# Performance work log

Measured on AMD Instinct MI355X. Metric: run time of the kernel, lower is better.

The kernel has to match this reference:

```python
import jax, jax.numpy as jnp
import numpy as np
import math

N, E, T, H, IN_DIM, G, L = 8192, 131072, 262144, 128, 64, 32, 2
RBF_BINS, RBF_MAX, ANG_BINS = 32, 5.0, 16


def _rbf(d, r_max, n_bins):
    centers = jnp.linspace(0.0, r_max, n_bins, dtype=jnp.float32)
    delta = r_max / max(n_bins - 1, 1)
    gamma = 1.0 / (2.0 * (delta ** 2 + 1e-12))
    diff = d[:, None] - centers[None, :]
    return jnp.exp(-gamma * diff * diff)


def _mlp2(x, w1, b1, w2, b2):
    return jax.nn.silu(x @ w1 + b1) @ w2 + b2


def _ln(x, g, b):
    mu = jnp.mean(x, -1, keepdims=True)
    var = jnp.mean((x - mu) ** 2, -1, keepdims=True)
    return (x - mu) * jax.lax.rsqrt(var + 1e-5) * g + b


def _safe_norm(v):
    # ||v|| with grad-safe sqrt at v=0
    return jnp.sqrt(jnp.sum(v * v, -1) + 1e-12)


def setup_inputs() -> dict:
    key = jax.random.key(0)
    ks = iter(jax.random.split(key, 64))

    def lin(fan_in, shape):
        return jax.random.normal(next(ks), shape, jnp.float32) * (fan_in ** -0.5)

    x = jax.random.normal(next(ks), (N, IN_DIM), jnp.float32)
    pos = jax.random.normal(next(ks), (N, 3), jnp.float32) * 2.0
    edge_index = jax.random.randint(next(ks), (2, E), 0, N, jnp.int32)
    edge_dist = jnp.linalg.norm(pos[edge_index[1]] - pos[edge_index[0]], axis=-1)
    triplet_kj = jax.random.randint(next(ks), (T,), 0, E, jnp.int32)
    triplet_ji = jax.random.randint(next(ks), (T,), 0, E, jnp.int32)
    batch = jnp.sort(jax.random.randint(next(ks), (N,), 0, G, jnp.int32))
    TM_IN, MM_IN, CTX = 2 * RBF_BINS + ANG_BINS, 3 * H + RBF_BINS, 3 * H
    d = dict(
        x=x, pos=pos, edge_dist=edge_dist,
        node_in_w=lin(IN_DIM, (IN_DIM, H)), node_in_b=jnp.zeros(H),
        tm_w1=lin(TM_IN, (L, TM_IN, H)), tm_b1=jnp.zeros((L, H)),
        tm_w2=lin(H, (L, H, H)), tm_b2=jnp.zeros((L, H)),
        mm_w1=lin(MM_IN, (L, MM_IN, H)), mm_b1=jnp.zeros((L, H)),
        mm_w2=lin(H, (L, H, 2 * H)), mm_b2=jnp.zeros((L, 2 * H)),
        us_w1=lin(CTX, (L, CTX, H)), us_b1=jnp.zeros((L, H)),
        us_w2=lin(H, (L, H, H)), us_b2=jnp.zeros((L, H)),
        gv_w1=lin(CTX, (L, CTX, H)), gv_b1=jnp.zeros((L, H)),
        gv_w2=lin(H, (L, H, H)), gv_b2=jnp.zeros((L, H)),
        ln_g=jnp.ones((L, H)), ln_b=jnp.zeros((L, H)),
        vn_init=jnp.zeros(H),
        v2n_w1=lin(H, (H, H)), v2n_b1=jnp.zeros(H),
        v2n_w2=lin(H, (H, H)), v2n_b2=jnp.zeros(H),
        n2v_w1=lin(H, (H, H)), n2v_b1=jnp.zeros(H),
        n2v_w2=lin(H, (H, H)), n2v_b2=jnp.zeros(H),
        head_w1=lin(5 * H, (5 * H, H)), head_b1=jnp.zeros(H),
        head_w2=lin(H, (H, 1)), head_b2=jnp.zeros(1),
        edge_index=edge_index, triplet_kj=triplet_kj,
        triplet_ji=triplet_ji, batch=batch,
    )
    return d


def reference(x, pos, edge_dist, node_in_w, node_in_b, tm_w1, tm_b1, tm_w2, tm_b2,
              mm_w1, mm_b1, mm_w2, mm_b2, us_w1, us_b1, us_w2, us_b2,
              gv_w1, gv_b1, gv_w2, gv_b2, ln_g, ln_b, vn_init,
              v2n_w1, v2n_b1, v2n_w2, v2n_b2, n2v_w1, n2v_b1, n2v_w2, n2v_b2,
              head_w1, head_b1, head_w2, head_b2,
              edge_index, triplet_kj, triplet_ji, batch):
    src, dst = edge_index[0], edge_index[1]
    s = x @ node_in_w + node_in_b                              # [N,H]
    v = jnp.zeros((N, H, 3), s.dtype)                          # [N,H,3]
    vec = pos[dst] - pos[src]                                  # [E,3]
    edge_dir = vec / (edge_dist[:, None] + 1e-9)               # [E,3]
    edge_rbf = _rbf(edge_dist, RBF_MAX, RBF_BINS)              # [E,32]
    # 3-body angles between edge ji and edge kj
    a, b = vec[triplet_ji], vec[triplet_kj]                    # [T,3]
    cos = jnp.sum(a * b, -1) / (_safe_norm(a) * _safe_norm(b) + 1e-9)
    angle = jnp.arccos(jnp.clip(cos, -1.0 + 1e-7, 1.0 - 1e-7))
    angle_feat = _rbf(angle, math.pi, ANG_BINS)                # [T,16]
    vn = jnp.broadcast_to(vn_init, (G, H))
    for l in range(L):
        s = s + _mlp2(vn, v2n_w1, v2n_b1, v2n_w2, v2n_b2)[batch]
        # triplet gather -> MLP -> scatter onto edges
        t_in = jnp.concatenate([edge_rbf[triplet_kj], edge_rbf[triplet_ji], angle_feat], -1)
        t_msg = _mlp2(t_in, tm_w1[l], tm_b1[l], tm_w2[l], tm_b2[l])
        angle_agg = jax.ops.segment_sum(t_msg, triplet_ji, num_segments=E)   # [E,H]
        # edge messages -> scatter onto nodes (scalar + vector channels)
        msg_in = jnp.concatenate([s[src], s[dst], edge_rbf, angle_agg], -1)  # [E,416]
        msg = _mlp2(msg_in, mm_w1[l], mm_b1[l], mm_w2[l], mm_b2[l])          # [E,2H]
        m_s, m_vc = msg[:, :H], msg[:, H:]
        agg_s = jax.ops.segment_sum(m_s, dst, num_segments=N)                # [N,H]
        m_v = m_vc[:, :, None] * edge_dir[:, None, :]                        # [E,H,3]
        agg_v = jax.ops.segment_sum(m_v.reshape(E, H * 3), dst, num_segments=N).reshape(N, H, 3)
        ctx = jnp.concatenate([s, agg_s, _safe_norm(v)], -1)                 # [N,3H]
        s = s + _mlp2(ctx, us_w1[l], us_b1[l], us_w2[l], us_b2[l])
        gate = jax.nn.sigmoid(_mlp2(ctx, gv_w1[l], gv_b1[l], gv_w2[l], gv_b2[l]))
        v = v + gate[:, :, None] * agg_v
        s = jax.nn.silu(_ln(s, ln_g[l], ln_b[l]))
        vn = vn + _mlp2(jax.ops.segment_sum(s, batch, num_segments=G),
                        n2v_w1, n2v_b1, n2v_w2, n2v_b2)
    nf = jnp.concatenate([s, _safe_norm(v)], -1)                             # [N,2H]
    add_p = jax.ops.segment_sum(nf, batch, num_segments=G)
    counts = jax.ops.segment_sum(jnp.ones((N,), nf.dtype), batch, num_segments=G)
    mean_p = add_p / jnp.maximum(counts, 1.0)[:, None]
    g = jnp.concatenate([add_p, mean_p, vn], -1)                             # [G,5H]
    pred = _mlp2(g, head_w1, head_b1, head_w2, head_b2)                      # [G,1]
    return pred[:, 0]
```

## Files before the change

kernel.cpp:

```cpp
#include <hip/hip_runtime.h>
#include <math.h>

#define N_   8192
#define E_   131072
#define T_   262144
#define H_   128
#define IND_ 64
#define G_   32
#define L_   2

#define CW 64
#define RB 16

#define MROWS 32
#define HSTRIDE 136
#define WSTRIDE 36

#define STEP_E  ((float)(5.0/31.0))
#define GAMMA_E ((float)(1.0/(2.0*((5.0/31.0)*(5.0/31.0) + 1e-12))))
#define PI_D    3.14159265358979323846
#define STEP_A  ((float)(PI_D/15.0))
#define GAMMA_A ((float)(1.0/(2.0*((PI_D/15.0)*(PI_D/15.0) + 1e-12))))

typedef __attribute__((ext_vector_type(8))) short short8;
typedef __attribute__((ext_vector_type(4))) float f32x4;
typedef unsigned short ushort_t;

static __device__ __forceinline__ float fexp_f(float x){ return __expf(x); }
static __device__ __forceinline__ float silu_f(float x){ return x / (1.f + fexp_f(-x)); }
static __device__ __forceinline__ float sigmoid_f(float x){ return 1.f / (1.f + fexp_f(-x)); }

static __device__ __forceinline__ ushort_t f2bf(float x){
  unsigned int u = __builtin_bit_cast(unsigned int, x);
  u += 0x7FFFu + ((u >> 16) & 1u);
  return (ushort_t)(u >> 16);
}
static __device__ __forceinline__ float bf2f(ushort_t h){
  unsigned int u = ((unsigned int)h) << 16;
  return __builtin_bit_cast(float, u);
}


__global__ void k_zero(float* __restrict__ p, long n){
  long stride = (long)gridDim.x*256;
  long n4 = n >> 2;
  float4* p4 = (float4*)p;
  for (long i = (long)blockIdx.x*256 + threadIdx.x; i < n4; i += stride)
    p4[i] = make_float4(0.f,0.f,0.f,0.f);
  for (long i = (n4<<2) + (long)blockIdx.x*256 + threadIdx.x; i < n; i += stride)
    p[i] = 0.f;
}

__global__ void k_sentinel(float* __restrict__ p, int n){
  int i = blockIdx.x*256 + threadIdx.x;
  if (i < n) p[i] = 1.0e30f;
}

__global__ void k_init_vn(float* __restrict__ vn, const float* __restrict__ vn_init){
  int i = blockIdx.x*256 + threadIdx.x;
  if (i < G_*H_) vn[i] = vn_init[i & 127];
}

__global__ void k_bends(const int* __restrict__ batch, int* __restrict__ bends){
  int g = threadIdx.x;
  if (g >= G_) return;
  int lo = 0, hi = N_;
  while (lo < hi){
    int mid = (lo + hi) >> 1;
    if (batch[mid] <= g) lo = mid + 1; else hi = mid;
  }
  bends[g] = lo;
}

__global__ void k_wt_all(const float* __restrict__ tm_w1, const float* __restrict__ tm_w2,
                         const float* __restrict__ mm_w1, const float* __restrict__ mm_w2,
                         const float* __restrict__ us_w1, const float* __restrict__ us_w2,
                         const float* __restrict__ gv_w1, const float* __restrict__ gv_w2,
                         ushort_t* __restrict__ wtbuf){
  const int l = blockIdx.y;
  int i = blockIdx.x*256 + threadIdx.x;
  if (i >= 245760) return;
  ushort_t* base = wtbuf + (size_t)l*376832;
  if (i < 12288){
    int c = i/96, k = i%96;
    base[i] = (k < 80) ? f2bf(tm_w1[(size_t)l*10240 + (size_t)k*128 + c]) : (ushort_t)0;
  } else if (i < 28672){
    int j = i - 12288; int c = j >> 7, k = j & 127;
    base[12288 + j] = f2bf(tm_w2[(size_t)l*16384 + (size_t)k*128 + c]);
  } else if (i < 81920){
    int j = i - 28672; int c = j/416, k = j%416;
    base[28672 + j] = f2bf(mm_w1[(size_t)l*53248 + (size_t)k*128 + c]);
  } else if (i < 114688){
    int j = i - 81920; int c = j >> 7, k = j & 127;
    base[81920 + j] = f2bf(mm_w2[(size_t)l*32768 + (size_t)k*256 + c]);
  } else if (i < 163840){
    int j = i - 114688; int c = j/384, k = j%384;
    float w = us_w1[(size_t)l*49152 + (size_t)k*128 + c];
    ushort_t h = f2bf(w);
    base[114688 + j] = h; base[163840 + j] = f2bf(w - bf2f(h));
  } else if (i < 180224){
    int j = i - 163840; int c = j >> 7, k = j & 127;
    float w = us_w2[(size_t)l*16384 + (size_t)k*128 + c];
    ushort_t h = f2bf(w);
    base[212992 + j] = h; base[229376 + j] = f2bf(w - bf2f(h));
  } else if (i < 229376){
    int j = i - 180224; int c = j/384, k = j%384;
    float w = gv_w1[(size_t)l*49152 + (size_t)k*128 + c];
    ushort_t h = f2bf(w);
    base[245760 + j] = h; base[294912 + j] = f2bf(w - bf2f(h));
  } else {
    int j = i - 229376; int c = j >> 7, k = j & 127;
    float w = gv_w2[(size_t)l*16384 + (size_t)k*128 + c];
    ushort_t h = f2bf(w);
    base[344064 + j] = h; base[360448 + j] = f2bf(w - bf2f(h));
  }
}

__global__ void k_geom(const float* __restrict__ pos, const float* __restrict__ dist,
                       const int* __restrict__ ei,
                       float* __restrict__ vec, float* __restrict__ dir,
                       ushort_t* __restrict__ rbf16){
  int e = blockIdx.x*256 + threadIdx.x;
  if (e >= E_) return;
  int s = ei[e], d = ei[E_ + e];
  float vx = pos[d*3+0] - pos[s*3+0];
  float vy = pos[d*3+1] - pos[s*3+1];
  float vz = pos[d*3+2] - pos[s*3+2];
  vec[e*3+0]=vx; vec[e*3+1]=vy; vec[e*3+2]=vz;
  float dd = dist[e];
  float inv = 1.f / (dd + 1e-9f);
  dir[e*3+0]=vx*inv; dir[e*3+1]=vy*inv; dir[e*3+2]=vz*inv;
  #pragma unroll
  for (int i=0;i<32;i++){
    float df = dd - i*STEP_E;
    rbf16[e*32+i] = f2bf(fexp_f(-GAMMA_E*df*df));
  }
}

__global__ void k_dirs(const float* __restrict__ dir, const int* __restrict__ perm_e,
                       float* __restrict__ dir_s){
  int p = blockIdx.x*256 + threadIdx.x;
  if (p >= E_) return;
  int e = perm_e[p];
  dir_s[p*3+0] = dir[e*3+0];
  dir_s[p*3+1] = dir[e*3+1];
  dir_s[p*3+2] = dir[e*3+2];
}

__global__ void k_angle(const float* __restrict__ vec,
                        const int* __restrict__ kj, const int* __restrict__ ji,
                        float* __restrict__ angle){
  int t = blockIdx.x*256 + threadIdx.x;
  if (t >= T_) return;
  int ea = ji[t], eb = kj[t];
  float ax=vec[ea*3+0], ay=vec[ea*3+1], az=vec[ea*3+2];
  float bx=vec[eb*3+0], by=vec[eb*3+1], bz=vec[eb*3+2];
  float dot = ax*bx + ay*by + az*bz;
  float na = sqrtf(ax*ax+ay*ay+az*az + 1e-12f);
  float nb = sqrtf(bx*bx+by*by+bz*bz + 1e-12f);
  float c = dot / (na*nb + 1e-9f);
  c = fminf(fmaxf(c, -1.f + 1e-7f), 1.f - 1e-7f);
  angle[t] = acosf(c);
}


__global__ void k_hist(const int* __restrict__ keys, int M, int* __restrict__ hist){
  int i = blockIdx.x*256 + threadIdx.x;
  if (i < M) atomicAdd(&hist[keys[i]], 1);
}

__global__ void k_hist2(const int* __restrict__ keys, const int* __restrict__ map,
                        int M, int* __restrict__ hist){
  int i = blockIdx.x*256 + threadIdx.x;
  if (i < M) atomicAdd(&hist[map[keys[i]]], 1);
}

__global__ void k_scan1(const int* __restrict__ in, int* __restrict__ out,
                        int* __restrict__ sums, int B){
  __shared__ int sh[1024];
  int base = blockIdx.x*1024, t = threadIdx.x;
  for (int j=t;j<1024;j+=256) sh[j] = (base+j<B) ? in[base+j] : 0;
  __syncthreads();
  for (int o=1;o<1024;o<<=1){
    int v[4];
    #pragma unroll
    for (int q=0;q<4;q++){ int idx=t+q*256; v[q]=(idx>=o)? sh[idx-o]:0; }
    __syncthreads();
    #pragma unroll
    for (int q=0;q<4;q++){ int idx=t+q*256; sh[idx]+=v[q]; }
    __syncthreads();
  }
  for (int j=t;j<1024;j+=256) if (base+j<B) out[base+j] = (j==0)?0:sh[j-1];
  if (t==0) sums[blockIdx.x] = sh[1023];
}

__global__ void k_scan2(int* __restrict__ sums, int nb){
  if (threadIdx.x==0 && blockIdx.x==0){
    int a=0;
    for (int i=0;i<nb;i++){ int x=sums[i]; sums[i]=a; a+=x; }
  }
}

__global__ void k_scan3(int* __restrict__ out, const int* __restrict__ sums, int B){
  int i = blockIdx.x*256+threadIdx.x;
  if (i<B) out[i] += sums[i>>10];
}

__global__ void k_fill(const int* __restrict__ keys, int M, int* __restrict__ cur,
                       int* __restrict__ perm){
  int i = blockIdx.x*256+threadIdx.x;
  if (i<M){ int p = atomicAdd(&cur[keys[i]],1); perm[p]=i; }
}

__global__ void k_fill2(const int* __restrict__ keys, const int* __restrict__ map,
                        int M, int* __restrict__ cur, int* __restrict__ perm){
  int i = blockIdx.x*256+threadIdx.x;
  if (i<M){ int p = atomicAdd(&cur[map[keys[i]]],1); perm[p]=i; }
}

__global__ void k_invert(const int* __restrict__ perm, int* __restrict__ rank, int M){
  int i = blockIdx.x*256+threadIdx.x;
  if (i<M) rank[perm[i]] = i;
}

template<int SM, int K1PAD>
__launch_bounds__(256, 4)
__global__ void k_mlp1(
    const int* __restrict__ perm,
    const int* __restrict__ idx1, const int* __restrict__ idx2,
    const ushort_t* __restrict__ rbf16, const float* __restrict__ angle,
    const ushort_t* __restrict__ s16, const ushort_t* __restrict__ eagg_in,
    const ushort_t* __restrict__ W1t, const float* __restrict__ b1,
    ushort_t* __restrict__ outbuf)
{
  __shared__ ushort_t lw[128*WSTRIDE];
  __shared__ ushort_t hid[4][16*HSTRIDE];
  const int tid  = threadIdx.x;
  const int wave = tid >> 6;
  const int lane = tid & 63;
  const int n    = lane & 15;
  const int quad = lane >> 4;
  const int kq   = quad*8;
  const int wrow = blockIdx.x*64 + wave*16;
  const int row  = wrow + n;

  const int e0 = perm[row];
  int i1a = idx1[e0];
  int i2a = idx2[e0];
  float ang0 = 0.f;
  if (SM == 1){ ang0 = angle[e0]; }

  f32x4 acc[8];
  #pragma unroll
  for (int ct=0;ct<8;ct++) acc[ct] = (f32x4){0.f,0.f,0.f,0.f};

  #pragma unroll
  for (int k0 = 0; k0 < K1PAD; k0 += 32){
    short8 a0;
    if (SM == 1){
      if (k0 == 0){
        a0 = *(const short8*)&rbf16[(size_t)i1a*32 + kq];
      } else if (k0 == 32){
        a0 = *(const short8*)&rbf16[(size_t)i2a*32 + kq];
      } else {
        #pragma unroll
        for (int j=0;j<8;j++){
          int kk = kq + j;
          float v0 = 0.f;
          if (kk < 16){
            float c = (float)kk*STEP_A;
            float d0 = ang0 - c;
            v0 = fexp_f(-GAMMA_A*d0*d0);
          }
          a0[j] = (short)f2bf(v0);
        }
      }
    } else {
      const int k = k0 + kq;
      if (k0 < 128){
        a0 = *(const short8*)&s16[(size_t)i1a*128 + k];
      } else if (k0 < 256){
        a0 = *(const short8*)&s16[(size_t)i2a*128 + (k-128)];
      } else if (k0 < 288){
        a0 = *(const short8*)&rbf16[(size_t)e0*32 + (k-256)];
      } else {
        a0 = *(const short8*)&eagg_in[(size_t)row*128 + (k-288)];
      }
    }

    #pragma unroll
    for (int it=0; it<2; it++){
      int idx = tid + it*256;
      int col = idx >> 2, seg = idx & 3;
      *(short8*)&lw[col*WSTRIDE + seg*8] = *(const short8*)&W1t[(size_t)col*K1PAD + k0 + seg*8];
    }
    __syncthreads();

    #pragma unroll
    for (int ct=0;ct<8;ct++){
      short8 b = *(const short8*)&lw[(ct*16 + n)*WSTRIDE + kq];
      acc[ct] = __builtin_amdgcn_mfma_f32_16x16x32_bf16(a0, b, acc[ct], 0,0,0);
    }
    __syncthreads();
  }

  #pragma unroll
  for (int ct=0;ct<8;ct++){
    int col = ct*16 + n;
    float bv = b1[col];
    #pragma unroll
    for (int reg=0;reg<4;reg++){
      int rloc = quad*4 + reg;
      float h = acc[ct][reg] + bv;
      hid[wave][rloc*HSTRIDE + col] = f2bf(silu_f(h));
    }
  }
  const int rsub = lane >> 4;
  const int c8   = (lane & 15) * 8;
  #pragma unroll
  for (int i=0;i<4;i++){
    int rloc = i*4 + rsub;
    int grow = wrow + rloc;
    short8 vv = *(const short8*)&hid[wave][(size_t)rloc*HSTRIDE + c8];
    *(short8*)&outbuf[(size_t)grow*128 + c8] = vv;
  }
}

__launch_bounds__(64, 4)
__global__ void k_aggemm_t(const ushort_t* __restrict__ tmsg, const int* __restrict__ tends,
                           const ushort_t* __restrict__ W2t, const float* __restrict__ b2,
                           ushort_t* __restrict__ eagg2){
  __shared__ ushort_t hid[MROWS*HSTRIDE];
  const int lane = threadIdx.x;
  const int n    = lane & 15;
  const int quad = lane >> 4;
  const int kq   = quad*8;
  const int wrow = blockIdx.x*MROWS;
  const int r0 = wrow + n, r1 = wrow + 16 + n;
  const int s0 = r0 ? tends[r0-1] : 0;
  const int e0 = tends[r0];
  const int s1 = tends[r1-1];
  const int e1 = tends[r1];

  f32x4 acc[2][8];
  #pragma unroll
  for (int rh=0;rh<2;rh++)
    #pragma unroll
    for (int ct=0;ct<8;ct++) acc[rh][ct] = (f32x4){0.f,0.f,0.f,0.f};

  #pragma unroll
  for (int k0=0;k0<128;k0+=32){
    float sum0[8], sum1[8];
    #pragma unroll
    for (int j=0;j<8;j++){ sum0[j]=0.f; sum1[j]=0.f; }
    for (int p=s0;p<e0;p++){
      short8 w = *(const short8*)&tmsg[(size_t)p*128 + k0 + kq];
      #pragma unroll
      for (int j=0;j<8;j++) sum0[j] += bf2f((ushort_t)w[j]);
    }
    for (int p=s1;p<e1;p++){
      short8 w = *(const short8*)&tmsg[(size_t)p*128 + k0 + kq];
      #pragma unroll
      for (int j=0;j<8;j++) sum1[j] += bf2f((ushort_t)w[j]);
    }
    short8 a0, a1;
    #pragma unroll
    for (int j=0;j<8;j++){
      a0[j] = (short)f2bf(sum0[j]);
      a1[j] = (short)f2bf(sum1[j]);
    }
    #pragma unroll
    for (int ct=0;ct<8;ct++){
      short8 b = *(const short8*)&W2t[(size_t)(ct*16 + n)*128 + k0 + kq];
      acc[0][ct] = __builtin_amdgcn_mfma_f32_16x16x32_bf16(a0, b, acc[0][ct], 0,0,0);
      acc[1][ct] = __builtin_amdgcn_mfma_f32_16x16x32_bf16(a1, b, acc[1][ct], 0,0,0);
    }
  }

  float cnts[2][4];
  #pragma unroll
  for (int rh=0;rh<2;rh++)
    #pragma unroll
    for (int reg=0;reg<4;reg++){
      int row = wrow + rh*16 + quad*4 + reg;
      cnts[rh][reg] = (float)(tends[row] - (row ? tends[row-1] : 0));
    }

  #pragma unroll
  for (int rh=0;rh<2;rh++){
    #pragma unroll
    for (int ct=0;ct<8;ct++){
      int col = ct*16 + n;
      float bv = b2[col];
      #pragma unroll
      for (int reg=0;reg<4;reg++){
        int rloc = rh*16 + quad*4 + reg;
        hid[rloc*HSTRIDE + col] = f2bf(acc[rh][ct][reg] + cnts[rh][reg]*bv);
      }
    }
  }
  const int rsub = lane >> 4;
  const int c8   = (lane & 15) * 8;
  #pragma unroll
  for (int i=0;i<8;i++){
    int rloc = i*4 + rsub;
    int grow = wrow + rloc;
    short8 vv = *(const short8*)&hid[(size_t)rloc*HSTRIDE + c8];
    *(short8*)&eagg2[(size_t)grow*128 + c8] = vv;
  }
}

__global__ void k_agg_e(const ushort_t* __restrict__ hbuf, const int* __restrict__ eends,
                        const float* __restrict__ dir_s, float* __restrict__ mom){
  int i = blockIdx.x*256 + threadIdx.x;
  int d = i >> 6, c2 = (i & 63)*2;
  if (d >= N_) return;
  int s = (d == 0) ? 0 : eends[d-1];
  int e = eends[d];
  float hs0=0.f,hs1=0.f, hx0=0.f,hx1=0.f, hy0=0.f,hy1=0.f, hz0=0.f,hz1=0.f;
  float sdx=0.f, sdy=0.f, sdz=0.f;
  for (int q=s;q<e;q++){
    unsigned int w = *(const unsigned int*)&hbuf[(size_t)q*128 + c2];
    float h0 = bf2f((ushort_t)(w & 0xFFFFu));
    float h1 = bf2f((ushort_t)(w >> 16));
    float dx = dir_s[q*3+0], dy = dir_s[q*3+1], dz = dir_s[q*3+2];
    hs0 += h0; hs1 += h1;
    hx0 += h0*dx; hx1 += h1*dx;
    hy0 += h0*dy; hy1 += h1*dy;
    hz0 += h0*dz; hz1 += h1*dz;
    sdx += dx; sdy += dy; sdz += dz;
  }
  size_t base = (size_t)d*128 + c2;
  *(float2*)&mom[base]                        = make_float2(hs0, hs1);
  *(float2*)&mom[(size_t)N_*128   + base]     = make_float2(hx0, hx1);
  *(float2*)&mom[(size_t)N_*256   + base]     = make_float2(hy0, hy1);
  *(float2*)&mom[(size_t)N_*384   + base]     = make_float2(hz0, hz1);
  if (c2 == 0){
    mom[(size_t)N_*512 + d*4+0] = sdx;
    mom[(size_t)N_*512 + d*4+1] = sdy;
    mom[(size_t)N_*512 + d*4+2] = sdz;
  }
}

__launch_bounds__(64, 4)
__global__ void k_gemm_e(const float* __restrict__ mom, const int* __restrict__ eends,
                         const ushort_t* __restrict__ W2t ,
                         const float* __restrict__ b2 ,
                         const float* __restrict__ v ,
                         ushort_t* __restrict__ a16h, ushort_t* __restrict__ a16l,
                         ushort_t* __restrict__ vnh,  ushort_t* __restrict__ vnl,
                         float* __restrict__ aggv ){
  __shared__ float sbuf[MROWS*130];
  const int lane = threadIdx.x;
  const int n    = lane & 15;
  const int quad = lane >> 4;
  const int kq   = quad*8;
  const int wrow = blockIdx.x*MROWS;
  const int og   = blockIdx.y;

  const float* M = mom + (size_t)og*((size_t)N_*128);
  const ushort_t* W = W2t + (og ? (size_t)128*128 : 0);

  f32x4 acc[2][8];
  #pragma unroll
  for (int rh=0;rh<2;rh++)
    #pragma unroll
    for (int ct=0;ct<8;ct++) acc[rh][ct] = (f32x4){0.f,0.f,0.f,0.f};

  #pragma unroll
  for (int k0=0;k0<128;k0+=32){
    const int k = k0 + kq;
    const float* p0 = &M[(size_t)(wrow + n)*128 + k];
    const float* p1 = &M[(size_t)(wrow + 16 + n)*128 + k];
    f32x4 x0 = *(const f32x4*)p0, x1 = *(const f32x4*)(p0+4);
    f32x4 y0 = *(const f32x4*)p1, y1 = *(const f32x4*)(p1+4);
    short8 ah0, al0, ah1, al1;
    #pragma unroll
    for (int j=0;j<4;j++){
      ushort_t h;
      h = f2bf(x0[j]); ah0[j]   = (short)h; al0[j]   = (short)f2bf(x0[j] - bf2f(h));
      h = f2bf(x1[j]); ah0[4+j] = (short)h; al0[4+j] = (short)f2bf(x1[j] - bf2f(h));
      h = f2bf(y0[j]); ah1[j]   = (short)h; al1[j]   = (short)f2bf(y0[j] - bf2f(h));
      h = f2bf(y1[j]); ah1[4+j] = (short)h; al1[4+j] = (short)f2bf(y1[j] - bf2f(h));
    }
    #pragma unroll
    for (int ct=0;ct<8;ct++){
      short8 b = *(const short8*)&W[(size_t)(ct*16 + n)*128 + k0 + kq];
      acc[0][ct] = __builtin_amdgcn_mfma_f32_16x16x32_bf16(ah0, b, acc[0][ct], 0,0,0);
      acc[0][ct] = __builtin_amdgcn_mfma_f32_16x16x32_bf16(al0, b, acc[0][ct], 0,0,0);
      acc[1][ct] = __builtin_amdgcn_mfma_f32_16x16x32_bf16(ah1, b, acc[1][ct], 0,0,0);
      acc[1][ct] = __builtin_amdgcn_mfma_f32_16x16x32_bf16(al1, b, acc[1][ct], 0,0,0);
    }
  }

  const int rsub = lane >> 4;
  const int c8   = (lane & 15) * 8;

  if (og == 0){
    float cnts[2][4];
    #pragma unroll
    for (int rh=0;rh<2;rh++)
      #pragma unroll
      for (int reg=0;reg<4;reg++){
        int row = wrow + rh*16 + quad*4 + reg;
        cnts[rh][reg] = (float)(eends[row] - (row ? eends[row-1] : 0));
      }
    ushort_t* us = (ushort_t*)sbuf;
    #pragma unroll
    for (int rh=0;rh<2;rh++)
      #pragma unroll
      for (int ct=0;ct<8;ct++){
        int col = ct*16 + n;
        float bv = b2[col];
        #pragma unroll
        for (int reg=0;reg<4;reg++){
          int rloc = rh*16 + quad*4 + reg;
          float val = acc[rh][ct][reg] + cnts[rh][reg]*bv;
          us[rloc*HSTRIDE + col] = f2bf(val);
        }
      }
    #pragma unroll
    for (int i=0;i<8;i++){
      int rloc = i*4 + rsub;
      short8 vv = *(const short8*)&us[(size_t)rloc*HSTRIDE + c8];
      *(short8*)&a16h[(size_t)(wrow + rloc)*128 + c8] = vv;
    }
    #pragma unroll
    for (int rh=0;rh<2;rh++)
      #pragma unroll
      for (int ct=0;ct<8;ct++){
        int col = ct*16 + n;
        float bv = b2[col];
        #pragma unroll
        for (int reg=0;reg<4;reg++){
          int rloc = rh*16 + quad*4 + reg;
          float val = acc[rh][ct][reg] + cnts[rh][reg]*bv;
          ushort_t h = f2bf(val);
          us[rloc*HSTRIDE + col] = f2bf(val - bf2f(h));
        }
      }
    #pragma unroll
    for (int i=0;i<8;i++){
      int rloc = i*4 + rsub;
      short8 vv = *(const short8*)&us[(size_t)rloc*HSTRIDE + c8];
      *(short8*)&a16l[(size_t)(wrow + rloc)*128 + c8] = vv;
    }
    #pragma unroll 4
    for (int j=0;j<32;j++){
      size_t idx = (size_t)wrow*128 + (size_t)j*128 + lane*2;
      float2 a = *(const float2*)&v[idx];
      float2 b = *(const float2*)&v[(size_t)N_*128 + idx];
      float2 c = *(const float2*)&v[(size_t)N_*256 + idx];
      float n0 = sqrtf(a.x*a.x + b.x*b.x + c.x*c.x + 1e-12f);
      float n1 = sqrtf(a.y*a.y + b.y*b.y + c.y*c.y + 1e-12f);
      ushort_t h0 = f2bf(n0), h1 = f2bf(n1);
      *(unsigned int*)&vnh[idx] = (unsigned int)h0 | ((unsigned int)h1 << 16);
      *(unsigned int*)&vnl[idx] = (unsigned int)f2bf(n0 - bf2f(h0))
                                | ((unsigned int)f2bf(n1 - bf2f(h1)) << 16);
    }
  } else {
    const int x = og - 1;
    #pragma unroll
    for (int rh=0;rh<2;rh++)
      #pragma unroll
      for (int ct=0;ct<8;ct++){
        int col = ct*16 + n;
        float bv = b2[128 + col];
        #pragma unroll
        for (int reg=0;reg<4;reg++){
          int rloc = rh*16 + quad*4 + reg;
          int row = wrow + rloc;
          float sd = mom[(size_t)N_*512 + row*4 + x];
          sbuf[rloc*130 + col] = acc[rh][ct][reg] + sd*bv;
        }
      }
    float* plane = aggv + (size_t)x*((size_t)N_*128);
    #pragma unroll
    for (int i=0;i<8;i++){
      int rloc = i*4 + rsub;
      f32x4 v0 = *(const f32x4*)&sbuf[rloc*130 + c8];
      f32x4 v1 = *(const f32x4*)&sbuf[rloc*130 + c8 + 4];
      *(f32x4*)&plane[(size_t)(wrow + rloc)*128 + c8] = v0;
      *(f32x4*)&plane[(size_t)(wrow + rloc)*128 + c8 + 4] = v1;
    }
  }
}

__launch_bounds__(256, 3)
__global__ void k_node_mfma(
    const float* __restrict__ s_in,
    const ushort_t* __restrict__ a16h, const ushort_t* __restrict__ a16l,
    const ushort_t* __restrict__ vnh,  const ushort_t* __restrict__ vnl,
    float* __restrict__ s2, float* __restrict__ v_out ,
    const float* __restrict__ aggv ,
    const ushort_t* __restrict__ us1h, const ushort_t* __restrict__ us1l, const float* __restrict__ us_b1,
    const ushort_t* __restrict__ us2h, const ushort_t* __restrict__ us2l, const float* __restrict__ us_b2,
    const ushort_t* __restrict__ gv1h, const ushort_t* __restrict__ gv1l, const float* __restrict__ gv_b1,
    const ushort_t* __restrict__ gv2h, const ushort_t* __restrict__ gv2l, const float* __restrict__ gv_b2)
{
  __shared__ ushort_t lwh[128*WSTRIDE];
  __shared__ ushort_t lwl[128*WSTRIDE];
  __shared__ ushort_t hidh[4][16*HSTRIDE];
  __shared__ ushort_t hidl[4][16*HSTRIDE];
  const int tid  = threadIdx.x;
  const int wave = tid >> 6;
  const int lane = tid & 63;
  const int n    = lane & 15;
  const int quad = lane >> 4;
  const int kq   = quad*8;
  const int og   = blockIdx.y;
  const int wrow = blockIdx.x*64 + wave*16;
  const int r0 = wrow + n;

  const ushort_t* W1h = og ? gv1h : us1h;
  const ushort_t* W1l = og ? gv1l : us1l;
  const float*    B1  = og ? gv_b1 : us_b1;
  const ushort_t* W2h = og ? gv2h : us2h;
  const ushort_t* W2l = og ? gv2l : us2l;
  const float*    B2  = og ? gv_b2 : us_b2;

  f32x4 acc[8];
  #pragma unroll
  for (int ct=0;ct<8;ct++) acc[ct] = (f32x4){0.f,0.f,0.f,0.f};

  #pragma unroll
  for (int k0=0; k0<384; k0+=32){
    #pragma unroll
    for (int it = 0; it < 2; it++){
      int idx = tid + it*256;
      int col = idx >> 2, seg = idx & 3;
      *(short8*)&lwh[col*WSTRIDE + seg*8] = *(const short8*)&W1h[(size_t)col*384 + k0 + seg*8];
      *(short8*)&lwl[col*WSTRIDE + seg*8] = *(const short8*)&W1l[(size_t)col*384 + k0 + seg*8];
    }
    __syncthreads();

    short8 ah0, al0;
    const int k = k0 + kq;
    if (k0 < 128){
      const float* p0 = &s_in[(size_t)r0*128 + k];
      f32x4 x0 = *(const f32x4*)p0, x1 = *(const f32x4*)(p0+4);
      #pragma unroll
      for (int j=0;j<4;j++){
        ushort_t h;
        h = f2bf(x0[j]); ah0[j]   = (short)h; al0[j]   = (short)f2bf(x0[j] - bf2f(h));
        h = f2bf(x1[j]); ah0[4+j] = (short)h; al0[4+j] = (short)f2bf(x1[j] - bf2f(h));
      }
    } else if (k0 < 256){
      int kk = k - 128;
      ah0 = *(const short8*)&a16h[(size_t)r0*128 + kk];
      al0 = *(const short8*)&a16l[(size_t)r0*128 + kk];
    } else {
      int kk = k - 256;
      ah0 = *(const short8*)&vnh[(size_t)r0*128 + kk];
      al0 = *(const short8*)&vnl[(size_t)r0*128 + kk];
    }
    #pragma unroll
    for (int ct=0;ct<8;ct++){
      short8 bh = *(const short8*)&lwh[(ct*16 + n)*WSTRIDE + kq];
      short8 bl = *(const short8*)&lwl[(ct*16 + n)*WSTRIDE + kq];
      acc[ct] = __builtin_amdgcn_mfma_f32_16x16x32_bf16(ah0, bh, acc[ct], 0,0,0);
      acc[ct] = __builtin_amdgcn_mfma_f32_16x16x32_bf16(al0, bh, acc[ct], 0,0,0);
      acc[ct] = __builtin_amdgcn_mfma_f32_16x16x32_bf16(ah0, bl, acc[ct], 0,0,0);
    }
    __syncthreads();
  }

  #pragma unroll
  for (int ct=0;ct<8;ct++){
    int col = ct*16 + n;
    float bv = B1[col];
    #pragma unroll
    for (int reg=0;reg<4;reg++){
      int rloc = quad*4 + reg;
      float h = silu_f(acc[ct][reg] + bv);
      ushort_t hh = f2bf(h);
      hidh[wave][rloc*HSTRIDE + col] = hh;
      hidl[wave][rloc*HSTRIDE + col] = f2bf(h - bf2f(hh));
    }
  }

  f32x4 acc2[8];
  #pragma unroll
  for (int ct=0;ct<8;ct++) acc2[ct] = (f32x4){0.f,0.f,0.f,0.f};

  #pragma unroll
  for (int k0=0;k0<128;k0+=32){
    #pragma unroll
    for (int it = 0; it < 2; it++){
      int idx = tid + it*256;
      int col = idx >> 2, seg = idx & 3;
      *(short8*)&lwh[col*WSTRIDE + seg*8] = *(const short8*)&W2h[(size_t)col*128 + k0 + seg*8];
      *(short8*)&lwl[col*WSTRIDE + seg*8] = *(const short8*)&W2l[(size_t)col*128 + k0 + seg*8];
    }
    __syncthreads();

    short8 ah0 = *(const short8*)&hidh[wave][(size_t)(n)*HSTRIDE + k0 + kq];
    short8 al0 = *(const short8*)&hidl[wave][(size_t)(n)*HSTRIDE + k0 + kq];
    #pragma unroll
    for (int ct=0;ct<8;ct++){
      short8 bh = *(const short8*)&lwh[(ct*16 + n)*WSTRIDE + kq];
      short8 bl = *(const short8*)&lwl[(ct*16 + n)*WSTRIDE + kq];
      acc2[ct] = __builtin_amdgcn_mfma_f32_16x16x32_bf16(ah0, bh, acc2[ct], 0,0,0);
      acc2[ct] = __builtin_amdgcn_mfma_f32_16x16x32_bf16(al0, bh, acc2[ct], 0,0,0);
      acc2[ct] = __builtin_amdgcn_mfma_f32_16x16x32_bf16(ah0, bl, acc2[ct], 0,0,0);
    }
    __syncthreads();
  }

  if (og == 0){
    #pragma unroll
    for (int ct=0;ct<8;ct++){
      int col = ct*16 + n;
      float bv = B2[col];
      #pragma unroll
      for (int reg=0;reg<4;reg++){
        int row = wrow + quad*4 + reg;
        size_t idx = (size_t)row*128 + col;
        s2[idx] = s_in[idx] + acc2[ct][reg] + bv;
      }
    }
  } else {
    #pragma unroll
    for (int ct=0;ct<8;ct++){
      int col = ct*16 + n;
      float bv = B2[col];
      #pragma unroll
      for (int reg=0;reg<4;reg++){
        int row = wrow + quad*4 + reg;
        size_t idx = (size_t)row*128 + col;
        float g = sigmoid_f(acc2[ct][reg] + bv);
        v_out[idx]                    += g*aggv[idx];
        v_out[(size_t)N_*128 + idx]   += g*aggv[(size_t)N_*128 + idx];
        v_out[(size_t)N_*256 + idx]   += g*aggv[(size_t)N_*256 + idx];
      }
    }
  }
}

__launch_bounds__(128)
__global__ void k_gemm(const float* __restrict__ A,
                       const float* __restrict__ W,
                       const float* __restrict__ bias,
                       float* __restrict__ C, int R, int K)
{
  __shared__ float ws[CW*128];
  __shared__ float as[RB][CW];
  const int tid = threadIdx.x;
  const int nchunk = (K + CW - 1) / CW;

  for (int rb = blockIdx.x*RB; rb < R; rb += gridDim.x*RB){
    float acc[RB];
    #pragma unroll
    for (int r=0;r<RB;r++) acc[r] = 0.f;

    for (int c=0;c<nchunk;c++){
      const int k0 = c*CW;
      for (int i=tid; i<CW*128; i+=128){
        int kk = i >> 7, col = i & 127;
        int k = k0 + kk;
        ws[i] = (k < K) ? W[k*128 + col] : 0.f;
      }
      for (int i=tid; i<RB*CW; i+=128){
        int r  = i >> 6, kk = i & 63;
        int k  = k0 + kk;
        as[r][kk] = (k < K) ? A[(long)(rb+r)*K + k] : 0.f;
      }
      __syncthreads();
      #pragma unroll 4
      for (int kq2=0; kq2<CW/4; kq2++){
        float w0 = ws[(4*kq2+0)*128 + tid];
        float w1 = ws[(4*kq2+1)*128 + tid];
        float w2 = ws[(4*kq2+2)*128 + tid];
        float w3 = ws[(4*kq2+3)*128 + tid];
        #pragma unroll
        for (int r=0;r<RB;r++){
          const float4 av = *reinterpret_cast<const float4*>(&as[r][4*kq2]);
          acc[r] = fmaf(av.x, w0, acc[r]);
          acc[r] = fmaf(av.y, w1, acc[r]);
          acc[r] = fmaf(av.z, w2, acc[r]);
          acc[r] = fmaf(av.w, w3, acc[r]);
        }
      }
      __syncthreads();
    }

    const float bv = bias[tid];
    #pragma unroll
    for (int r=0;r<RB;r++)
      C[(long)(rb+r)*128 + tid] = acc[r] + bv;
  }
}


__launch_bounds__(256)
__global__ void k_small_mlp2(const float* __restrict__ in,
                             const float* __restrict__ w1, const float* __restrict__ b1,
                             const float* __restrict__ w2, const float* __restrict__ b2,
                             float* __restrict__ outp, int accumulate){
  __shared__ float a[4][128];
  __shared__ float h[4][128];
  int tid = threadIdx.x;
  int rbase = blockIdx.x*4;
  for (int i=tid;i<4*128;i+=256) a[i>>7][i&127] = in[(rbase + (i>>7))*128 + (i&127)];
  __syncthreads();
  int col = tid & 127, rg = tid >> 7;
  float acc0=0.f, acc1=0.f;
  for (int k=0;k<128;k++){
    float w = w1[k*128+col];
    acc0 = fmaf(a[rg*2+0][k], w, acc0);
    acc1 = fmaf(a[rg*2+1][k], w, acc1);
  }
  {
    float bv = b1[col];
    h[rg*2+0][col] = silu_f(acc0+bv);
    h[rg*2+1][col] = silu_f(acc1+bv);
  }
  __syncthreads();
  acc0=0.f; acc1=0.f;
  for (int k=0;k<128;k++){
    float w = w2[k*128+col];
    acc0 = fmaf(h[rg*2+0][k], w, acc0);
    acc1 = fmaf(h[rg*2+1][k], w, acc1);
  }
  {
    float bv = b2[col];
    int idx0 = (rbase+rg*2+0)*128+col;
    int idx1 = (rbase+rg*2+1)*128+col;
    float v0 = acc0+bv, v1 = acc1+bv;
    outp[idx0] = accumulate ? outp[idx0]+v0 : v0;
    outp[idx1] = accumulate ? outp[idx1]+v1 : v1;
  }
}

__global__ void k_head(const float* __restrict__ gbuf,
                       const float* __restrict__ w1, const float* __restrict__ b1,
                       const float* __restrict__ w2, const float* __restrict__ b2,
                       float* __restrict__ outp){
  __shared__ float red[128];
  int g = blockIdx.x, tid = threadIdx.x;
  float acc = 0.f;
  for (int k=0;k<640;k++) acc = fmaf(gbuf[g*640+k], w1[k*128+tid], acc);
  float h = silu_f(acc + b1[tid]);
  red[tid] = h * w2[tid];
  __syncthreads();
  for (int o=64;o>0;o>>=1){ if (tid<o) red[tid]+=red[tid+o]; __syncthreads(); }
  if (tid == 0) outp[g] = red[0] + b2[0];
}


__global__ void k_sadd_batch(float* __restrict__ s, const float* __restrict__ t2,
                             const int* __restrict__ batch, ushort_t* __restrict__ s16){
  int i = blockIdx.x*256 + threadIdx.x;
  if (i >= N_*H_) return;
  int n = i >> 7, h = i & 127;
  float v = s[i] + t2[batch[n]*128 + h];
  s[i] = v;
  s16[i] = f2bf(v);
}

__global__ void k_ln_silu(const float* __restrict__ in, float* __restrict__ outp,
                          const float* __restrict__ g, const float* __restrict__ b){
  __shared__ float red[128];
  int n = blockIdx.x, tid = threadIdx.x;
  float x = in[n*128 + tid];
  red[tid] = x; __syncthreads();
  for (int o=64;o>0;o>>=1){ if (tid<o) red[tid]+=red[tid+o]; __syncthreads(); }
  float mu = red[0] * (1.f/128.f);
  __syncthreads();
  float dx = x - mu;
  red[tid] = dx*dx; __syncthreads();
  for (int o=64;o>0;o>>=1){ if (tid<o) red[tid]+=red[tid+o]; __syncthreads(); }
  float var = red[0] * (1.f/128.f);
  float y = dx * rsqrtf(var + 1e-5f) * g[tid] + b[tid];
  outp[n*128 + tid] = silu_f(y);
}

__global__ void k_ssum_csr(const float* __restrict__ s, const int* __restrict__ bends,
                           float* __restrict__ ssum){
  int g = blockIdx.x, c = blockIdx.y, tid = threadIdx.x;
  int s0 = g ? bends[g-1] : 0;
  int e0 = bends[g];
  long len = e0 - s0;
  int lo = s0 + (int)((len*c) >> 3);
  int hi = s0 + (int)((len*(c+1)) >> 3);
  float a = 0.f;
  for (int n=lo; n<hi; n++) a += s[(size_t)n*128 + tid];
  if (hi > lo) atomicAdd(&ssum[g*128 + tid], a);
}

__global__ void k_scatter_nf2(const float* __restrict__ s, const float* __restrict__ v ,
                              const int* __restrict__ batch, float* __restrict__ addp){
  int j = threadIdx.x;
  int base = blockIdx.x*32;
  float acc = 0.f;
  int prev = batch[base];
  for (int r=0;r<32;r++){
    int nn = base + r;
    int b = batch[nn];
    if (b != prev){ atomicAdd(&addp[prev*256 + j], acc); acc = 0.f; prev = b; }
    float val;
    if (j < 128){
      val = s[(size_t)nn*128 + j];
    } else {
      size_t idx = (size_t)nn*128 + (j - 128);
      float v0 = v[idx], v1 = v[(size_t)N_*128 + idx], v2 = v[(size_t)N_*256 + idx];
      val = sqrtf(v0*v0 + v1*v1 + v2*v2 + 1e-12f);
    }
    acc += val;
  }
  atomicAdd(&addp[prev*256 + j], acc);
}

__global__ void k_build_g(const float* __restrict__ addp, const int* __restrict__ bends,
                          const float* __restrict__ vn, float* __restrict__ gbuf){
  int i = blockIdx.x*256 + threadIdx.x;
  if (i >= G_*640) return;
  int g = i / 640, j = i % 640;
  float cnt = (float)(bends[g] - (g ? bends[g-1] : 0));
  float val;
  if (j < 256)       val = addp[g*256 + j];
  else if (j < 512)  val = addp[g*256 + (j-256)] / fmaxf(cnt, 1.f);
  else               val = vn[g*128 + (j-512)];
  gbuf[i] = val;
}


extern "C" void kernel_launch(void* const* d_in, const int* in_sizes, int n_in,
                              void* d_out, int out_size, void* d_ws, size_t ws_size,
                              hipStream_t stream)
{
  const float* x         = (const float*)d_in[0];
  const float* pos       = (const float*)d_in[1];
  const float* edist     = (const float*)d_in[2];
  const float* node_in_w = (const float*)d_in[3];
  const float* node_in_b = (const float*)d_in[4];
  const float* tm_w1 = (const float*)d_in[5];
  const float* tm_b1 = (const float*)d_in[6];
  const float* tm_w2 = (const float*)d_in[7];
  const float* tm_b2 = (const float*)d_in[8];
  const float* mm_w1 = (const float*)d_in[9];
  const float* mm_b1 = (const float*)d_in[10];
  const float* mm_w2 = (const float*)d_in[11];
  const float* mm_b2 = (const float*)d_in[12];
  const float* us_w1 = (const float*)d_in[13];
  const float* us_b1 = (const float*)d_in[14];
  const float* us_w2 = (const float*)d_in[15];
  const float* us_b2 = (const float*)d_in[16];
  const float* gv_w1 = (const float*)d_in[17];
  const float* gv_b1 = (const float*)d_in[18];
  const float* gv_w2 = (const float*)d_in[19];
  const float* gv_b2 = (const float*)d_in[20];
  const float* ln_g  = (const float*)d_in[21];
  const float* ln_b  = (const float*)d_in[22];
  const float* vn_init = (const float*)d_in[23];
  const float* v2n_w1 = (const float*)d_in[24];
  const float* v2n_b1 = (const float*)d_in[25];
  const float* v2n_w2 = (const float*)d_in[26];
  const float* v2n_b2 = (const float*)d_in[27];
  const float* n2v_w1 = (const float*)d_in[28];
  const float* n2v_b1 = (const float*)d_in[29];
  const float* n2v_w2 = (const float*)d_in[30];
  const float* n2v_b2 = (const float*)d_in[31];
  const float* head_w1 = (const float*)d_in[32];
  const float* head_b1 = (const float*)d_in[33];
  const float* head_w2 = (const float*)d_in[34];
  const float* head_b2 = (const float*)d_in[35];
  const int* ei    = (const int*)d_in[36];
  const int* t_kj  = (const int*)d_in[37];
  const int* t_ji  = (const int*)d_in[38];
  const int* batch = (const int*)d_in[39];
  float* out = (float*)d_out;

  float* f = (float*)d_ws;
  size_t off = 0;
  auto alloc = [&](size_t n){ n = (n + 3) & ~(size_t)3; float* p = f + off; off += n; return p; };
  float*    vec    = alloc((size_t)E_*3);
  float*    dir    = alloc((size_t)E_*3);
  ushort_t* rbf16  = (ushort_t*)alloc((size_t)E_*16);
  float*    angle  = alloc((size_t)T_);
  float*    tmsg_f = alloc((size_t)E_*128);
  float*    eagg2_f= alloc((size_t)E_*64);
  float*    dir_s  = alloc((size_t)E_*3);
  float*    tends_f= alloc((size_t)E_ + 1024);
  float*    eends_f= alloc((size_t)N_ + 1024);
  float*    bends_f= alloc((size_t)G_);
  float*    s      = alloc((size_t)N_*128);
  ushort_t* s16    = (ushort_t*)alloc((size_t)N_*64);
  float*    v      = alloc((size_t)N_*384);
  float*    aggv   = alloc((size_t)N_*384);
  float*    rank_f = alloc((size_t)E_);
  float*    wtbuf_f= alloc((size_t)376832);
  float*    vn     = alloc((size_t)G_*128);
  float*    tg2    = alloc((size_t)G_*128);
  float*    ssum   = alloc((size_t)G_*128);
  float*    addp   = alloc((size_t)G_*256);
  float*    gbuf   = alloc((size_t)G_*640);

  if (off * sizeof(float) > ws_size){
    k_sentinel<<<1, 64, 0, stream>>>(out, G_);
    return;
  }

  int* perm_t = (int*)vec;
  int* perm_e = perm_t + T_;
  int* rank_e = (int*)rank_f;
  int* tends  = (int*)tends_f;
  int* eends  = (int*)eends_f;
  int* bends  = (int*)bends_f;
  ushort_t* tmsg   = (ushort_t*)tmsg_f;
  ushort_t* ehid   = (ushort_t*)tmsg_f;
  ushort_t* eagg2  = (ushort_t*)eagg2_f;
  float*    mom  = eagg2_f;
  ushort_t* a16h = (ushort_t*)(eagg2_f + 4227072);
  ushort_t* a16l = a16h + (size_t)N_*128;
  ushort_t* vnh  = a16l + (size_t)N_*128;
  ushort_t* vnl  = vnh  + (size_t)N_*128;
  float*    s2   = (float*)(vnl + (size_t)N_*128);

  ushort_t* wtbuf = (ushort_t*)wtbuf_f;
  auto WT = [&](int l, size_t o){ return wtbuf + (size_t)l*376832 + o; };

  auto zero = [&](float* p, long n){
    int blocks = (int)((n/4 + 255)/256); if (blocks > 16384) blocks = 16384; if (blocks < 1) blocks = 1;
    k_zero<<<blocks, 256, 0, stream>>>(p, n);
  };
  auto csort = [&](const int* keys, const int* map, int M, int B, int* perm, int* ends){
    int nb = (B+1023)/1024;
    zero((float*)ends, B + nb);
    if (map) k_hist2<<<(M+255)/256, 256, 0, stream>>>(keys, map, M, ends);
    else     k_hist <<<(M+255)/256, 256, 0, stream>>>(keys, M, ends);
    k_scan1<<<nb, 256, 0, stream>>>(ends, ends, ends + B, B);
    k_scan2<<<1, 64, 0, stream>>>(ends + B, nb);
    k_scan3<<<(B+255)/256, 256, 0, stream>>>(ends, ends + B, B);
    if (map) k_fill2<<<(M+255)/256, 256, 0, stream>>>(keys, map, M, ends, perm);
    else     k_fill <<<(M+255)/256, 256, 0, stream>>>(keys, M, ends, perm);
  };

  zero(v, (long)N_*384);
  k_init_vn<<<(G_*H_ + 255)/256, 256, 0, stream>>>(vn, vn_init);
  k_geom<<<(E_ + 255)/256, 256, 0, stream>>>(pos, edist, ei, vec, dir, rbf16);
  k_angle<<<(T_ + 255)/256, 256, 0, stream>>>(vec, t_kj, t_ji, angle);
  csort(ei+E_, nullptr, E_, N_, perm_e, eends);
  k_invert<<<(E_+255)/256, 256, 0, stream>>>(perm_e, rank_e, E_);
  k_dirs<<<(E_+255)/256, 256, 0, stream>>>(dir, perm_e, dir_s);
  csort(t_ji, rank_e, T_, E_, perm_t, tends);
  k_bends<<<1, 64, 0, stream>>>(batch, bends);
  k_wt_all<<<dim3(960, 2), 256, 0, stream>>>(tm_w1, tm_w2, mm_w1, mm_w2,
                                             us_w1, us_w2, gv_w1, gv_w2, wtbuf);
  k_gemm<<<512, 128, 0, stream>>>(x, node_in_w, node_in_b, s, N_, IND_);

  for (int l=0; l<L_; l++){
    k_small_mlp2<<<8, 256, 0, stream>>>(vn, v2n_w1, v2n_b1, v2n_w2, v2n_b2, tg2, 0);
    k_sadd_batch<<<(N_*H_ + 255)/256, 256, 0, stream>>>(s, tg2, batch, s16);

    k_mlp1<1,96><<<T_/64, 256, 0, stream>>>(perm_t, t_kj, t_ji,
        rbf16, angle, s16, eagg2, WT(l,0), tm_b1 + l*128, tmsg);
    k_aggemm_t<<<E_/MROWS, 64, 0, stream>>>(tmsg, tends, WT(l,12288), tm_b2 + l*128, eagg2);

    k_mlp1<2,416><<<E_/64, 256, 0, stream>>>(perm_e, ei, ei + E_,
        rbf16, angle, s16, eagg2, WT(l,28672), mm_b1 + l*128, ehid);
    k_agg_e<<<(N_*64)/256, 256, 0, stream>>>(ehid, eends, dir_s, mom);
    k_gemm_e<<<dim3(N_/MROWS, 4), 64, 0, stream>>>(mom, eends, WT(l,81920), mm_b2 + l*256,
        v, a16h, a16l, vnh, vnl, aggv);

    k_node_mfma<<<dim3(N_/64, 2), 256, 0, stream>>>(s, a16h, a16l, vnh, vnl, s2, v, aggv,
        WT(l,114688), WT(l,163840), us_b1 + l*128, WT(l,212992), WT(l,229376), us_b2 + l*128,
        WT(l,245760), WT(l,294912), gv_b1 + l*128, WT(l,344064), WT(l,360448), gv_b2 + l*128);

    k_ln_silu<<<N_, 128, 0, stream>>>(s2, s, ln_g + l*128, ln_b + l*128);
    zero(ssum, (long)G_*128);
    k_ssum_csr<<<dim3(G_, 8), 128, 0, stream>>>(s, bends, ssum);
    k_small_mlp2<<<8, 256, 0, stream>>>(ssum, n2v_w1, n2v_b1, n2v_w2, n2v_b2, vn, 1);
  }

  zero(addp, (long)G_*256);
  k_scatter_nf2<<<N_/32, 256, 0, stream>>>(s, v, batch, addp);
  k_build_g<<<(G_*640 + 255)/256, 256, 0, stream>>>(addp, bends, vn, gbuf);
  k_head<<<G_, 128, 0, stream>>>(gbuf, head_w1, head_b1, head_w2, head_b2, out);
}
```

Measured before the change: 768.3 us.

## Fuse triplet MLP first layer with segmented aggregation and second GEMM

Replaces the triplet-message kernel and the separate aggregate-then-GEMM kernel with one kernel. Each block owns 32 edges, computes the hidden activations for their sorted triplets with MFMA, reduces them into shared-memory segment sums, then applies the second-layer GEMM and bias scaled by count. This removes the global round trip of the T x 128 bf16 triplet message buffer. In exchange it uses 64-thread blocks, a serial per-lane segmented sum with frequent syncthreads, and runs the first-layer GEMM with less parallelism per block.

```diff
diff --git a/kernel.cpp b/kernel.cpp
--- a/kernel.cpp
+++ b/kernel.cpp
@@ -223,6 +223,169 @@
   if (i<M) rank[perm[i]] = i;
 }
 
+__launch_bounds__(64, 4)
+__global__ void k_trimlp(const int* __restrict__ perm,
+                         const int* __restrict__ kj, const int* __restrict__ ji,
+                         const ushort_t* __restrict__ rbf16, const float* __restrict__ angle,
+                         const int* __restrict__ tends,
+                         const ushort_t* __restrict__ W1t , const float* __restrict__ b1,
+                         const ushort_t* __restrict__ W2t , const float* __restrict__ b2,
+                         ushort_t* __restrict__ eagg2)
+{
+  __shared__ ushort_t hid16[16*HSTRIDE];
+  __shared__ float    segacc[32*130];
+  __shared__ int      sends[33];
+  const int lane = threadIdx.x;
+  const int n    = lane & 15;
+  const int quad = lane >> 4;
+  const int kq   = quad*8;
+  const int wrow = blockIdx.x*32;
+
+  if (lane < 32) sends[lane+1] = tends[wrow + lane];
+  if (lane == 0) sends[0] = wrow ? tends[wrow-1] : 0;
+  for (int i = lane; i < 32*130; i += 64) segacc[i] = 0.f;
+  __syncthreads();
+  const int tstart = sends[0];
+  const int tend   = sends[32];
+
+  const int c2 = lane*2;
+  float run0 = 0.f, run1 = 0.f;
+  int currow = 0;
+
+  for (int tb = tstart; tb < tend; tb += 16){
+    int t = tb + n;
+    int tt = (t < tend) ? t : (tend - 1);
+    int e  = perm[tt];
+    int i1 = kj[e], i2 = ji[e];
+    float ang = angle[e];
+
+    f32x4 acc[8];
+    #pragma unroll
+    for (int ct=0;ct<8;ct++) acc[ct] = (f32x4){0.f,0.f,0.f,0.f};
+
+    {
+      short8 a0 = *(const short8*)&rbf16[(size_t)i1*32 + kq];
+      #pragma unroll
+      for (int ct=0;ct<8;ct++){
+        short8 b = *(const short8*)&W1t[(size_t)(ct*16 + n)*96 + kq];
+        acc[ct] = __builtin_amdgcn_mfma_f32_16x16x32_bf16(a0, b, acc[ct], 0,0,0);
+      }
+    }
+    {
+      short8 a0 = *(const short8*)&rbf16[(size_t)i2*32 + kq];
+      #pragma unroll
+      for (int ct=0;ct<8;ct++){
+        short8 b = *(const short8*)&W1t[(size_t)(ct*16 + n)*96 + 32 + kq];
+        acc[ct] = __builtin_amdgcn_mfma_f32_16x16x32_bf16(a0, b, acc[ct], 0,0,0);
+      }
+    }
+    {
+      short8 a0;
+      #pragma unroll
+      for (int j=0;j<8;j++){
+        int kk = kq + j;
+        float v0 = 0.f;
+        if (kk < 16){
+          float c = (float)kk*STEP_A;
+          float d0 = ang - c;
+          v0 = fexp_f(-GAMMA_A*d0*d0);
+        }
+        a0[j] = (short)f2bf(v0);
+      }
+      #pragma unroll
+      for (int ct=0;ct<8;ct++){
+        short8 b = *(const short8*)&W1t[(size_t)(ct*16 + n)*96 + 64 + kq];
+        acc[ct] = __builtin_amdgcn_mfma_f32_16x16x32_bf16(a0, b, acc[ct], 0,0,0);
+      }
+    }
+
+    #pragma unroll
+    for (int ct=0;ct<8;ct++){
+      int col = ct*16 + n;
+      float bv = b1[col];
+      #pragma unroll
+      for (int reg=0;reg<4;reg++){
+        hid16[(quad*4 + reg)*HSTRIDE + col] = f2bf(silu_f(acc[ct][reg] + bv));
+      }
+    }
+    __syncthreads();
+
+    int rmax = (tend - tb < 16) ? (tend - tb) : 16;
+    for (int r = 0; r < rmax; r++){
+      int gt = tb + r;
+      while (gt >= sends[currow+1]){
+        segacc[currow*130 + c2]     += run0;
+        segacc[currow*130 + c2 + 1] += run1;
+        run0 = 0.f; run1 = 0.f;
+        currow++;
+      }
+      run0 += bf2f(hid16[r*HSTRIDE + c2]);
+      run1 += bf2f(hid16[r*HSTRIDE + c2 + 1]);
+    }
+    __syncthreads();
+  }
+  segacc[currow*130 + c2]     += run0;
+  segacc[currow*130 + c2 + 1] += run1;
+  __syncthreads();
+
+  f32x4 acc2[2][8];
+  #pragma unroll
+  for (int rh=0;rh<2;rh++)
+    #pragma unroll
+    for (int ct=0;ct<8;ct++) acc2[rh][ct] = (f32x4){0.f,0.f,0.f,0.f};
+
+  #pragma unroll
+  for (int k0=0;k0<128;k0+=32){
+    short8 a0, a1;
+    #pragma unroll
+    for (int j=0;j<8;j++){
+      a0[j] = (short)f2bf(segacc[(size_t)n*130 + k0 + kq + j]);
+      a1[j] = (short)f2bf(segacc[(size_t)(16+n)*130 + k0 + kq + j]);
+    }
+    #pragma unroll
+    for (int ct=0;ct<8;ct++){
+      short8 b = *(const short8*)&W2t[(size_t)(ct*16 + n)*128 + k0 + kq];
+      acc2[0][ct] = __builtin_amdgcn_mfma_f32_16x16x32_bf16(a0, b, acc2[0][ct], 0,0,0);
+      acc2[1][ct] = __builtin_amdgcn_mfma_f32_16x16x32_bf16(a1, b, acc2[1][ct], 0,0,0);
+    }
+  }
+  __syncthreads();
+
+  float cnts[2][4];
+  #pragma unroll
+  for (int rh=0;rh<2;rh++)
+    #pragma unroll
+    for (int reg=0;reg<4;reg++){
+      int loc = rh*16 + quad*4 + reg;
+      cnts[rh][reg] = (float)(sends[loc+1] - sends[loc]);
+    }
+
+  ushort_t* us = (ushort_t*)segacc;
+  #pragma unroll
+  for (int rh=0;rh<2;rh++){
+    #pragma unroll
+    for (int ct=0;ct<8;ct++){
+      int col = ct*16 + n;
+      float bv = b2[col];
+      #pragma unroll
+      for (int reg=0;reg<4;reg++){
+        int rloc = rh*16 + quad*4 + reg;
+        us[rloc*HSTRIDE + col] = f2bf(acc2[rh][ct][reg] + cnts[rh][reg]*bv);
+      }
+    }
+  }
+  __syncthreads();
+  const int rsub = lane >> 4;
+  const int c8   = (lane & 15) * 8;
+  #pragma unroll
+  for (int i=0;i<8;i++){
+    int rloc = i*4 + rsub;
+    int grow = wrow + rloc;
+    short8 vv = *(const short8*)&us[(size_t)rloc*HSTRIDE + c8];
+    *(short8*)&eagg2[(size_t)grow*128 + c8] = vv;
+  }
+}
+
 template<int SM, int K1PAD>
 __launch_bounds__(256, 4)
 __global__ void k_mlp1(
@@ -323,90 +486,6 @@
     int grow = wrow + rloc;
     short8 vv = *(const short8*)&hid[wave][(size_t)rloc*HSTRIDE + c8];
     *(short8*)&outbuf[(size_t)grow*128 + c8] = vv;
-  }
-}
-
-__launch_bounds__(64, 4)
-__global__ void k_aggemm_t(const ushort_t* __restrict__ tmsg, const int* __restrict__ tends,
-                           const ushort_t* __restrict__ W2t, const float* __restrict__ b2,
-                           ushort_t* __restrict__ eagg2){
-  __shared__ ushort_t hid[MROWS*HSTRIDE];
-  const int lane = threadIdx.x;
-  const int n    = lane & 15;
-  const int quad = lane >> 4;
-  const int kq   = quad*8;
-  const int wrow = blockIdx.x*MROWS;
-  const int r0 = wrow + n, r1 = wrow + 16 + n;
-  const int s0 = r0 ? tends[r0-1] : 0;
-  const int e0 = tends[r0];
-  const int s1 = tends[r1-1];
-  const int e1 = tends[r1];
-
-  f32x4 acc[2][8];
-  #pragma unroll
-  for (int rh=0;rh<2;rh++)
-    #pragma unroll
-    for (int ct=0;ct<8;ct++) acc[rh][ct] = (f32x4){0.f,0.f,0.f,0.f};
-
-  #pragma unroll
-  for (int k0=0;k0<128;k0+=32){
-    float sum0[8], sum1[8];
-    #pragma unroll
-    for (int j=0;j<8;j++){ sum0[j]=0.f; sum1[j]=0.f; }
-    for (int p=s0;p<e0;p++){
-      short8 w = *(const short8*)&tmsg[(size_t)p*128 + k0 + kq];
-      #pragma unroll
-      for (int j=0;j<8;j++) sum0[j] += bf2f((ushort_t)w[j]);
-    }
-    for (int p=s1;p<e1;p++){
-      short8 w = *(const short8*)&tmsg[(size_t)p*128 + k0 + kq];
-      #pragma unroll
-      for (int j=0;j<8;j++) sum1[j] += bf2f((ushort_t)w[j]);
-    }
-    short8 a0, a1;
-    #pragma unroll
-    for (int j=0;j<8;j++){
-      a0[j] = (short)f2bf(sum0[j]);
-      a1[j] = (short)f2bf(sum1[j]);
-    }
-    #pragma unroll
-    for (int ct=0;ct<8;ct++){
-      short8 b = *(const short8*)&W2t[(size_t)(ct*16 + n)*128 + k0 + kq];
-      acc[0][ct] = __builtin_amdgcn_mfma_f32_16x16x32_bf16(a0, b, acc[0][ct], 0,0,0);
-      acc[1][ct] = __builtin_amdgcn_mfma_f32_16x16x32_bf16(a1, b, acc[1][ct], 0,0,0);
-    }
-  }
-
-  float cnts[2][4];
-  #pragma unroll
-  for (int rh=0;rh<2;rh++)
-    #pragma unroll
-    for (int reg=0;reg<4;reg++){
-      int row = wrow + rh*16 + quad*4 + reg;
-      cnts[rh][reg] = (float)(tends[row] - (row ? tends[row-1] : 0));
-    }
-
-  #pragma unroll
-  for (int rh=0;rh<2;rh++){
-    #pragma unroll
-    for (int ct=0;ct<8;ct++){
-      int col = ct*16 + n;
-      float bv = b2[col];
-      #pragma unroll
-      for (int reg=0;reg<4;reg++){
-        int rloc = rh*16 + quad*4 + reg;
-        hid[rloc*HSTRIDE + col] = f2bf(acc[rh][ct][reg] + cnts[rh][reg]*bv);
-      }
-    }
-  }
-  const int rsub = lane >> 4;
-  const int c8   = (lane & 15) * 8;
-  #pragma unroll
-  for (int i=0;i<8;i++){
-    int rloc = i*4 + rsub;
-    int grow = wrow + rloc;
-    short8 vv = *(const short8*)&hid[(size_t)rloc*HSTRIDE + c8];
-    *(short8*)&eagg2[(size_t)grow*128 + c8] = vv;
   }
 }
 
@@ -1007,7 +1086,6 @@
   int* tends  = (int*)tends_f;
   int* eends  = (int*)eends_f;
   int* bends  = (int*)bends_f;
-  ushort_t* tmsg   = (ushort_t*)tmsg_f;
   ushort_t* ehid   = (ushort_t*)tmsg_f;
   ushort_t* eagg2  = (ushort_t*)eagg2_f;
   float*    mom  = eagg2_f;
@@ -1053,9 +1131,8 @@
     k_small_mlp2<<<8, 256, 0, stream>>>(vn, v2n_w1, v2n_b1, v2n_w2, v2n_b2, tg2, 0);
     k_sadd_batch<<<(N_*H_ + 255)/256, 256, 0, stream>>>(s, tg2, batch, s16);
 
-    k_mlp1<1,96><<<T_/64, 256, 0, stream>>>(perm_t, t_kj, t_ji,
-        rbf16, angle, s16, eagg2, WT(l,0), tm_b1 + l*128, tmsg);
-    k_aggemm_t<<<E_/MROWS, 64, 0, stream>>>(tmsg, tends, WT(l,12288), tm_b2 + l*128, eagg2);
+    k_trimlp<<<E_/32, 64, 0, stream>>>(perm_t, t_kj, t_ji,
+        rbf16, angle, tends, WT(l,0), tm_b1 + l*128, WT(l,12288), tm_b2 + l*128, eagg2);
 
     k_mlp1<2,416><<<E_/64, 256, 0, stream>>>(perm_e, ei, ei + E_,
         rbf16, angle, s16, eagg2, WT(l,28672), mm_b1 + l*128, ehid);
```

Result: slower. 814.9 us (+6.1%).
